# Optimization experiments

Hardware: AMD Instinct MI355X
Metric: run time of the kernel (lower is better)

Reference implementation:

```python
import jax, jax.numpy as jnp
import numpy as np

B, C_IN, C_OUT = 8, 64, 64
H, W = 256, 256
FH, FW = 16, 16  # patch grid from weight map spatial dims
HYPER_PARAMS = C_OUT * C_IN  # kernel_size=1, groups=1


def setup_inputs() -> dict:
    key = jax.random.key(0)
    kx, ks = jax.random.split(key)
    x = jax.random.normal(kx, (B, C_IN, H, W), dtype=jnp.float32)
    # s is the hypernetwork-generated per-patch weight map [b, out*in, fh, fw]
    s = jax.random.normal(ks, (B, HYPER_PARAMS, FH, FW), dtype=jnp.float32)
    return {"x": x, "s": s}


def reference(x, s):
    b, c, h, w = x.shape
    fh, fw = s.shape[-2], s.shape[-1]
    ph, pw = h // fh, w // fw
    out_ch = s.shape[1] // c  # hyper_params = out_ch * c (1x1 kernel, groups=1)
    # weight.permute(0,2,3,1).reshape(b*fh*fw*out, in, 1, 1) -> per-patch [out, in]
    Wp = jnp.transpose(s, (0, 2, 3, 1)).reshape(b, fh, fw, out_ch, c)
    # x.view(b,c,fh,ph,fw,pw).permute(0,2,4,1,3,5) -> per-patch blocks [b,fh,fw,c,ph,pw]
    xp = jnp.transpose(x.reshape(b, c, fh, ph, fw, pw), (0, 2, 4, 1, 3, 5))
    # grouped 1x1 conv over b*fh*fw groups == batched small matmul per patch
    y = jnp.einsum('bijoc,bijcpq->bijopq', Wp, xp)
    # .view(b,fh,fw,-1,ph,pw).permute(0,3,1,4,2,5).reshape(b,-1,h,w)
    return jnp.transpose(y, (0, 3, 1, 4, 2, 5)).reshape(b, out_ch, h, w)
```

## Files before the change

kernel.cpp:

```cpp
#include <hip/hip_runtime.h>

#define NB 8
#define FH 16
#define FW 16

typedef __bf16 bf16x8 __attribute__((ext_vector_type(8)));
typedef float  f32x4  __attribute__((ext_vector_type(4)));

#define WS_BYTES ((size_t)NB * 256 * 512 * 16)

__global__ __launch_bounds__(256) void pack_w_kernel(
    const float* __restrict__ s, bf16x8* __restrict__ ws)
{
    __shared__ float lds[16 * 513];
    const int bid = blockIdx.x;
    const int b   = bid & 7;
    const int pi  = (bid >> 3) & 15;
    const int mt  = (bid >> 7) & 3;
    const int kk  = (bid >> 9) & 1;
    const int tid = threadIdx.x;

    #pragma unroll
    for (int pass = 0; pass < 8; ++pass) {
        const int idx   = pass * 256 + tid;
        const int u     = idx >> 2;
        const int pj4   = idx & 3;
        const int row16 = u >> 5;
        const int cc    = u & 31;
        const size_t row = (size_t)b * 4096 + mt * 1024 + row16 * 64 + kk * 32 + cc;
        const float4 v = *reinterpret_cast<const float4*>(
            s + row * 256 + pi * 16 + pj4 * 4);
        lds[(pj4 * 4 + 0) * 513 + cc * 16 + row16] = v.x;
        lds[(pj4 * 4 + 1) * 513 + cc * 16 + row16] = v.y;
        lds[(pj4 * 4 + 2) * 513 + cc * 16 + row16] = v.z;
        lds[(pj4 * 4 + 3) * 513 + cc * 16 + row16] = v.w;
    }
    __syncthreads();

    const int gl     = tid & 63;
    const int row16  = gl & 15;
    const int lanehi = gl >> 4;
    #pragma unroll
    for (int pjblk = 0; pjblk < 4; ++pjblk) {
        const int pj = pjblk * 4 + (tid >> 6);
        bf16x8 e;
        #pragma unroll
        for (int j = 0; j < 8; ++j)
            e[j] = (__bf16)lds[pj * 513 + (lanehi * 8 + j) * 16 + row16];
        ws[((size_t)(b * 256 + pi * 16 + pj)) * 512 + (mt * 2 + kk) * 64 + gl] = e;
    }
}

__global__ __launch_bounds__(256, 2) void gemm_kernel(
    const float* __restrict__ x,
    const bf16x8* __restrict__ ws,
    float* __restrict__ out)
{
    __shared__ char smem[32768];
    float* smemf = (float*)smem;

    const int bid = blockIdx.x;
    const int b   = bid & 7;
    const int pi  = (bid >> 3) & 15;
    const int ph  = (bid >> 7) & 1;
    const int pjp = (bid >> 8) & 7;
    const int t   = threadIdx.x;
    const int lane = t & 63;
    const int wv   = t >> 6;
    const int pat  = wv & 1;
    const int wrow = wv >> 1;
    const int q    = lane & 15;
    const int hi   = lane >> 4;
    const int w0   = pjp * 32;
    const int row0 = pi * 16 + ph * 8;

    const int swq = lane & 7;
    const int sco = lane >> 3;
    const float* xp0 = x + ((size_t)(b * 64 + sco * 8)) * 65536
                         + (size_t)(row0 + wv * 2) * 256 + w0 + swq * 4;
    f32x4 xv[16];
    #pragma unroll
    for (int pp = 0; pp < 2; ++pp)
        #pragma unroll
        for (int cc = 0; cc < 8; ++cc)
            xv[pp * 8 + cc] = *(const f32x4*)(xp0 + (size_t)cc * 65536
                                              + (size_t)pp * 256);

    const bf16x8* wbase = ws + ((size_t)(b * 256 + pi * 16 + pjp * 2 + pat)) * 512;
    bf16x8 a[4][2];
    #pragma unroll
    for (int mt = 0; mt < 4; ++mt)
        #pragma unroll
        for (int kk = 0; kk < 2; ++kk)
            a[mt][kk] = wbase[(mt * 2 + kk) * 64 + lane];

    __builtin_amdgcn_sched_barrier(0);

    #pragma unroll
    for (int pp = 0; pp < 2; ++pp) {
        const int p = wv * 2 + pp;
        #pragma unroll
        for (int i = 0; i < 4; ++i) {
            const int w = swq * 4 + i;
            bf16x8 e;
            #pragma unroll
            for (int cc = 0; cc < 8; ++cc)
                e[cc] = (__bf16)xv[pp * 8 + cc][i];
            *(bf16x8*)(smem + p * 4096 + w * 128
                       + ((sco * 16) ^ ((w & 7) << 4) ^ ((p & 7) << 4))) = e;
        }
    }
    __syncthreads();

    bf16x8 bfrag[4][2];
    #pragma unroll
    for (int nt = 0; nt < 4; ++nt) {
        const int p = wrow * 4 + nt;
        const int w = pat * 16 + q;
        #pragma unroll
        for (int kk = 0; kk < 2; ++kk) {
            const int co = kk * 4 + hi;
            bfrag[nt][kk] = *(const bf16x8*)(smem + p * 4096 + w * 128
                            + ((co * 16) ^ ((w & 7) << 4) ^ ((p & 7) << 4)));
        }
    }
    __syncthreads();

    const int u2t = t >> 3;
    const int wq2 = t & 7;
    #pragma unroll
    for (int h = 0; h < 2; ++h) {
        f32x4 acc[2][4];
        #pragma unroll
        for (int m2 = 0; m2 < 2; ++m2)
            #pragma unroll
            for (int nt = 0; nt < 4; ++nt)
                acc[m2][nt] = (f32x4){0.f, 0.f, 0.f, 0.f};

        #pragma unroll
        for (int m2 = 0; m2 < 2; ++m2) {
            const int mt = h * 2 + m2;
            #pragma unroll
            for (int nt = 0; nt < 4; ++nt) {
                acc[m2][nt] = __builtin_amdgcn_mfma_f32_16x16x32_bf16(
                    a[mt][0], bfrag[nt][0], acc[m2][nt], 0, 0, 0);
                acc[m2][nt] = __builtin_amdgcn_mfma_f32_16x16x32_bf16(
                    a[mt][1], bfrag[nt][1], acc[m2][nt], 0, 0, 0);
            }
        }

        #pragma unroll
        for (int m2 = 0; m2 < 2; ++m2)
            #pragma unroll
            for (int nt = 0; nt < 4; ++nt) {
                const int p = wrow * 4 + nt;
                #pragma unroll
                for (int r = 0; r < 4; ++r) {
                    const int o2 = m2 * 16 + hi * 4 + r;
                    const int w  = pat * 16 + q;
                    smemf[(o2 * 8 + p) * 32 + (w ^ ((o2 & 7) << 2))] = acc[m2][nt][r];
                }
            }
        __syncthreads();

        #pragma unroll
        for (int ps = 0; ps < 8; ++ps) {
            const int r2 = ps * 32 + u2t;
            const int o2 = r2 >> 3;
            const int p  = r2 & 7;
            f32x4 vv = *(const f32x4*)&smemf[(o2 * 8 + p) * 32
                                             + ((wq2 * 4) ^ ((o2 & 7) << 2))];
            *(f32x4*)(out + ((size_t)(b * 64 + h * 32 + o2)) * 65536
                          + (size_t)(row0 + p) * 256 + w0 + wq2 * 4) = vv;
        }
        if (h == 0) __syncthreads();
    }
}

__global__ __launch_bounds__(512) void hyperpatch_fallback(
    const float* __restrict__ x,
    const float* __restrict__ s,
    float* __restrict__ out)
{
    __shared__ bf16x8 afrag[2][512];
    const int bid = blockIdx.x;
    const int b   = bid >> 7;
    const int pi  = (bid >> 3) & 15;
    const int pj0 = (bid & 7) * 2;
    const int t   = threadIdx.x;
    const int lane = t & 63;
    const int wv   = t >> 6;

    {
        const int g  = t;
        const int mt = g >> 7;
        const int kk = (g >> 6) & 1;
        const int gl = g & 63;
        const int o  = mt * 16 + (gl & 15);
        const int c0 = kk * 32 + (gl >> 4) * 8;
        const float2* sb2 = reinterpret_cast<const float2*>(
            s + ((size_t)b * 4096) * 256 + pi * 16 + pj0);
        bf16x8 ta, tb;
        #pragma unroll
        for (int j = 0; j < 8; ++j) {
            float2 v = sb2[(size_t)(o * 64 + c0 + j) * 128];
            ta[j] = (__bf16)v.x;
            tb[j] = (__bf16)v.y;
        }
        afrag[0][g] = ta;
        afrag[1][g] = tb;
    }

    const int pat  = wv >> 2;
    const int wrow = wv & 3;
    const int q  = lane & 15;
    const int cb = (lane >> 4) * 8;
    const float* xbase = x + (((size_t)b * 64) * 256 + pi * 16) * 256
                           + (pj0 + pat) * 16 + q;
    bf16x8 bfrag[4][2];
    #pragma unroll
    for (int nt = 0; nt < 4; ++nt) {
        const int p = wrow * 4 + nt;
        #pragma unroll
        for (int kk = 0; kk < 2; ++kk) {
            const int c = kk * 32 + cb;
            bf16x8 tv;
            #pragma unroll
            for (int j = 0; j < 8; ++j) {
                float v = xbase[(size_t)(c + j) * 65536 + (size_t)p * 256];
                tv[j] = (__bf16)v;
            }
            bfrag[nt][kk] = tv;
        }
    }

    __syncthreads();

    bf16x8 a[4][2];
    #pragma unroll
    for (int mt = 0; mt < 4; ++mt)
        #pragma unroll
        for (int kk = 0; kk < 2; ++kk)
            a[mt][kk] = afrag[pat][(mt * 2 + kk) * 64 + lane];

    f32x4 acc[4][4];
    #pragma unroll
    for (int mt = 0; mt < 4; ++mt)
        #pragma unroll
        for (int nt = 0; nt < 4; ++nt)
            acc[mt][nt] = (f32x4){0.f, 0.f, 0.f, 0.f};

    #pragma unroll
    for (int mt = 0; mt < 4; ++mt) {
        #pragma unroll
        for (int nt = 0; nt < 4; ++nt) {
            acc[mt][nt] = __builtin_amdgcn_mfma_f32_16x16x32_bf16(
                a[mt][0], bfrag[nt][0], acc[mt][nt], 0, 0, 0);
            acc[mt][nt] = __builtin_amdgcn_mfma_f32_16x16x32_bf16(
                a[mt][1], bfrag[nt][1], acc[mt][nt], 0, 0, 0);
        }
    }

    const int ro = (lane >> 4) * 4;
    float* obase = out + (((size_t)b * 64) * 256 + pi * 16) * 256
                       + (pj0 + pat) * 16 + q;
    #pragma unroll
    for (int mt = 0; mt < 4; ++mt) {
        #pragma unroll
        for (int nt = 0; nt < 4; ++nt) {
            const int p = wrow * 4 + nt;
            #pragma unroll
            for (int r = 0; r < 4; ++r) {
                const int o = mt * 16 + ro + r;
                obase[(size_t)o * 65536 + (size_t)p * 256] = acc[mt][nt][r];
            }
        }
    }
}

extern "C" void kernel_launch(void* const* d_in, const int* in_sizes, int n_in,
                              void* d_out, int out_size, void* d_ws, size_t ws_size,
                              hipStream_t stream)
{
    (void)in_sizes; (void)n_in; (void)out_size;
    const float* x = (const float*)d_in[0];
    const float* s = (const float*)d_in[1];
    float* out = (float*)d_out;

    if (ws_size >= WS_BYTES && d_ws != nullptr) {
        bf16x8* ws = (bf16x8*)d_ws;
        pack_w_kernel<<<dim3(1024), dim3(256), 0, stream>>>(s, ws);
        gemm_kernel<<<dim3(2048), dim3(256), 0, stream>>>(x, ws, out);
    } else {
        hyperpatch_fallback<<<dim3(NB * FH * (FW / 2)), dim3(512), 0, stream>>>(x, s, out);
    }
}
```

Measured before the change: 74.21 us.

## Process both patch-row halves per block, prefetching second half during first compute

```diff
diff --git a/kernel.cpp b/kernel.cpp
--- a/kernel.cpp
+++ b/kernel.cpp
@@ -51,7 +51,7 @@
     }
 }
 
-__global__ __launch_bounds__(256, 2) void gemm_kernel(
+__global__ __launch_bounds__(256, 3) void gemm_kernel(
     const float* __restrict__ x,
     const bf16x8* __restrict__ ws,
     float* __restrict__ out)
@@ -62,8 +62,7 @@
     const int bid = blockIdx.x;
     const int b   = bid & 7;
     const int pi  = (bid >> 3) & 15;
-    const int ph  = (bid >> 7) & 1;
-    const int pjp = (bid >> 8) & 7;
+    const int pjp = (bid >> 7) & 7;
     const int t   = threadIdx.x;
     const int lane = t & 63;
     const int wv   = t >> 6;
@@ -72,19 +71,12 @@
     const int q    = lane & 15;
     const int hi   = lane >> 4;
     const int w0   = pjp * 32;
-    const int row0 = pi * 16 + ph * 8;
-
-    const int swq = lane & 7;
-    const int sco = lane >> 3;
-    const float* xp0 = x + ((size_t)(b * 64 + sco * 8)) * 65536
-                         + (size_t)(row0 + wv * 2) * 256 + w0 + swq * 4;
-    f32x4 xv[16];
-    #pragma unroll
-    for (int pp = 0; pp < 2; ++pp)
-        #pragma unroll
-        for (int cc = 0; cc < 8; ++cc)
-            xv[pp * 8 + cc] = *(const f32x4*)(xp0 + (size_t)cc * 65536
-                                              + (size_t)pp * 256);
+    const int swq  = lane & 7;
+    const int sco  = lane >> 3;
+    const int u2t  = t >> 3;
+    const int wq2  = t & 7;
+
+    const float* xrowbase = x + (size_t)(b * 64 + sco * 8) * 65536 + w0 + swq * 4;
 
     const bf16x8* wbase = ws + ((size_t)(b * 256 + pi * 16 + pjp * 2 + pat)) * 512;
     bf16x8 a[4][2];
@@ -94,8 +86,13 @@
         for (int kk = 0; kk < 2; ++kk)
             a[mt][kk] = wbase[(mt * 2 + kk) * 64 + lane];
 
-    __builtin_amdgcn_sched_barrier(0);
-
+    f32x4 xv[16];
+    #pragma unroll
+    for (int u = 0; u < 16; ++u) {
+        const int pp = u >> 3, cc = u & 7;
+        xv[u] = *(const f32x4*)(xrowbase + (size_t)cc * 65536
+                                + (size_t)(pi * 16 + wv * 2 + pp) * 256);
+    }
     #pragma unroll
     for (int pp = 0; pp < 2; ++pp) {
         const int p = wv * 2 + pp;
@@ -104,76 +101,105 @@
             const int w = swq * 4 + i;
             bf16x8 e;
             #pragma unroll
-            for (int cc = 0; cc < 8; ++cc)
-                e[cc] = (__bf16)xv[pp * 8 + cc][i];
+            for (int cc = 0; cc < 8; ++cc) e[cc] = (__bf16)xv[pp * 8 + cc][i];
             *(bf16x8*)(smem + p * 4096 + w * 128
                        + ((sco * 16) ^ ((w & 7) << 4) ^ ((p & 7) << 4))) = e;
         }
     }
     __syncthreads();
 
-    bf16x8 bfrag[4][2];
-    #pragma unroll
-    for (int nt = 0; nt < 4; ++nt) {
-        const int p = wrow * 4 + nt;
-        const int w = pat * 16 + q;
-        #pragma unroll
-        for (int kk = 0; kk < 2; ++kk) {
-            const int co = kk * 4 + hi;
-            bfrag[nt][kk] = *(const bf16x8*)(smem + p * 4096 + w * 128
-                            + ((co * 16) ^ ((w & 7) << 4) ^ ((p & 7) << 4)));
-        }
-    }
-    __syncthreads();
-
-    const int u2t = t >> 3;
-    const int wq2 = t & 7;
-    #pragma unroll
-    for (int h = 0; h < 2; ++h) {
-        f32x4 acc[2][4];
-        #pragma unroll
-        for (int m2 = 0; m2 < 2; ++m2)
-            #pragma unroll
-            for (int nt = 0; nt < 4; ++nt)
-                acc[m2][nt] = (f32x4){0.f, 0.f, 0.f, 0.f};
-
-        #pragma unroll
-        for (int m2 = 0; m2 < 2; ++m2) {
-            const int mt = h * 2 + m2;
-            #pragma unroll
-            for (int nt = 0; nt < 4; ++nt) {
-                acc[m2][nt] = __builtin_amdgcn_mfma_f32_16x16x32_bf16(
-                    a[mt][0], bfrag[nt][0], acc[m2][nt], 0, 0, 0);
-                acc[m2][nt] = __builtin_amdgcn_mfma_f32_16x16x32_bf16(
-                    a[mt][1], bfrag[nt][1], acc[m2][nt], 0, 0, 0);
-            }
-        }
-
-        #pragma unroll
-        for (int m2 = 0; m2 < 2; ++m2)
-            #pragma unroll
-            for (int nt = 0; nt < 4; ++nt) {
-                const int p = wrow * 4 + nt;
+    #pragma unroll
+    for (int ph = 0; ph < 2; ++ph) {
+        const int row0 = pi * 16 + ph * 8;
+
+        bf16x8 bfrag[4][2];
+        #pragma unroll
+        for (int nt = 0; nt < 4; ++nt) {
+            const int p = wrow * 4 + nt;
+            const int w = pat * 16 + q;
+            #pragma unroll
+            for (int kk = 0; kk < 2; ++kk) {
+                const int co = kk * 4 + hi;
+                bfrag[nt][kk] = *(const bf16x8*)(smem + p * 4096 + w * 128
+                                + ((co * 16) ^ ((w & 7) << 4) ^ ((p & 7) << 4)));
+            }
+        }
+        __syncthreads();
+
+        if (ph == 0) {
+            #pragma unroll
+            for (int u = 0; u < 16; ++u) {
+                const int pp = u >> 3, cc = u & 7;
+                xv[u] = *(const f32x4*)(xrowbase + (size_t)cc * 65536
+                                        + (size_t)(pi * 16 + 8 + wv * 2 + pp) * 256);
+            }
+            __builtin_amdgcn_sched_barrier(0);
+        }
+
+        #pragma unroll
+        for (int h = 0; h < 2; ++h) {
+            f32x4 acc[2][4];
+            #pragma unroll
+            for (int m2 = 0; m2 < 2; ++m2)
                 #pragma unroll
-                for (int r = 0; r < 4; ++r) {
-                    const int o2 = m2 * 16 + hi * 4 + r;
-                    const int w  = pat * 16 + q;
-                    smemf[(o2 * 8 + p) * 32 + (w ^ ((o2 & 7) << 2))] = acc[m2][nt][r];
+                for (int nt = 0; nt < 4; ++nt)
+                    acc[m2][nt] = (f32x4){0.f, 0.f, 0.f, 0.f};
+
+            #pragma unroll
+            for (int m2 = 0; m2 < 2; ++m2) {
+                const int mt = h * 2 + m2;
+                #pragma unroll
+                for (int nt = 0; nt < 4; ++nt) {
+                    acc[m2][nt] = __builtin_amdgcn_mfma_f32_16x16x32_bf16(
+                        a[mt][0], bfrag[nt][0], acc[m2][nt], 0, 0, 0);
+                    acc[m2][nt] = __builtin_amdgcn_mfma_f32_16x16x32_bf16(
+                        a[mt][1], bfrag[nt][1], acc[m2][nt], 0, 0, 0);
                 }
             }
-        __syncthreads();
-
-        #pragma unroll
-        for (int ps = 0; ps < 8; ++ps) {
-            const int r2 = ps * 32 + u2t;
-            const int o2 = r2 >> 3;
-            const int p  = r2 & 7;
-            f32x4 vv = *(const f32x4*)&smemf[(o2 * 8 + p) * 32
-                                             + ((wq2 * 4) ^ ((o2 & 7) << 2))];
-            *(f32x4*)(out + ((size_t)(b * 64 + h * 32 + o2)) * 65536
-                          + (size_t)(row0 + p) * 256 + w0 + wq2 * 4) = vv;
-        }
-        if (h == 0) __syncthreads();
+
+            #pragma unroll
+            for (int m2 = 0; m2 < 2; ++m2)
+                #pragma unroll
+                for (int nt = 0; nt < 4; ++nt) {
+                    const int p = wrow * 4 + nt;
+                    #pragma unroll
+                    for (int r = 0; r < 4; ++r) {
+                        const int o2 = m2 * 16 + hi * 4 + r;
+                        const int w  = pat * 16 + q;
+                        smemf[(o2 * 8 + p) * 32 + (w ^ ((o2 & 7) << 2))] = acc[m2][nt][r];
+                    }
+                }
+            __syncthreads();
+
+            #pragma unroll
+            for (int ps = 0; ps < 8; ++ps) {
+                const int r2 = ps * 32 + u2t;
+                const int o2 = r2 >> 3;
+                const int p  = r2 & 7;
+                f32x4 vv = *(const f32x4*)&smemf[(o2 * 8 + p) * 32
+                                                 + ((wq2 * 4) ^ ((o2 & 7) << 2))];
+                *(f32x4*)(out + (size_t)(b * 64 + h * 32 + o2) * 65536
+                              + (size_t)(row0 + p) * 256 + w0 + wq2 * 4) = vv;
+            }
+            __syncthreads();
+        }
+
+        if (ph == 0) {
+            #pragma unroll
+            for (int pp = 0; pp < 2; ++pp) {
+                const int p = wv * 2 + pp;
+                #pragma unroll
+                for (int i = 0; i < 4; ++i) {
+                    const int w = swq * 4 + i;
+                    bf16x8 e;
+                    #pragma unroll
+                    for (int cc = 0; cc < 8; ++cc) e[cc] = (__bf16)xv[pp * 8 + cc][i];
+                    *(bf16x8*)(smem + p * 4096 + w * 128
+                               + ((sco * 16) ^ ((w & 7) << 4) ^ ((p & 7) << 4))) = e;
+                }
+            }
+            __syncthreads();
+        }
     }
 }
 
@@ -290,7 +316,7 @@
     if (ws_size >= WS_BYTES && d_ws != nullptr) {
         bf16x8* ws = (bf16x8*)d_ws;
         pack_w_kernel<<<dim3(1024), dim3(256), 0, stream>>>(s, ws);
-        gemm_kernel<<<dim3(2048), dim3(256), 0, stream>>>(x, ws, out);
+        gemm_kernel<<<dim3(1024), dim3(256), 0, stream>>>(x, ws, out);
     } else {
         hyperpatch_fallback<<<dim3(NB * FH * (FW / 2)), dim3(512), 0, stream>>>(x, s, out);
     }
```

Measured after the change: 102.0 us. 1.37x slower.
